# Performance work log

Measured on AMD Instinct MI355X. Metric: run time of the kernel, lower is better.

## Reference

```python
import jax, jax.numpy as jnp
import numpy as np
import math

C_CURV = 1.0          # manifold curvature c
KH = KW = 3
STRIDE = (1, 1)
PADDING = (1, 1)
DILATION = (1, 1)
IN_CH = 64            # includes time channel
OUT_CH = 64           # excludes time channel


def setup_inputs() -> dict:
    key = jax.random.key(0)
    k1, k2, k3 = jax.random.split(key, 3)
    B, H, W = 32, 64, 64
    x = jax.random.normal(k1, (B, H, W, IN_CH), dtype=jnp.float32)
    kk = KH * KW
    lin_in = (IN_CH - 1) * kk + 1  # 568
    stdv = math.sqrt(2.0 / ((IN_CH - 1) * kk))
    weight = jax.random.uniform(k2, (OUT_CH, lin_in), minval=-stdv, maxval=stdv, dtype=jnp.float32)
    bias = jax.random.uniform(k3, (OUT_CH,), minval=-stdv, maxval=stdv, dtype=jnp.float32)
    return {"x": x, "weight": weight, "bias": bias}


def _im2col(x):
    """x: [B,H,W,C] -> gathered patches [B,h_out,w_out,KH,KW,C] (torch Unfold semantics)."""
    B, H, W, C = x.shape
    xp = jnp.pad(x, ((0, 0), (PADDING[0], PADDING[0]), (PADDING[1], PADDING[1]), (0, 0)))
    h_out = (H + 2 * PADDING[0] - DILATION[0] * (KH - 1) - 1) // STRIDE[0] + 1
    w_out = (W + 2 * PADDING[1] - DILATION[1] * (KW - 1) - 1) // STRIDE[1] + 1
    rows = STRIDE[0] * jnp.arange(h_out)[:, None] + DILATION[0] * jnp.arange(KH)[None, :]  # [h_out,KH]
    cols = STRIDE[1] * jnp.arange(w_out)[:, None] + DILATION[1] * jnp.arange(KW)[None, :]  # [w_out,KW]
    g = xp[:, rows[:, None, :, None], cols[None, :, None, :], :]  # [B,h_out,w_out,KH,KW,C]
    return g, h_out, w_out


def reference(x, weight, bias):
    B = x.shape[0]
    kk = KH * KW
    g, h_out, w_out = _im2col(x)
    L = h_out * w_out
    # Time channel (channel 0) over kernel positions, clamped to sqrt(c)
    t = jnp.maximum(g[..., 0].reshape(B, L, kk), jnp.sqrt(jnp.float32(C_CURV)))
    t_rescaled = jnp.sqrt(jnp.sum(t * t, axis=-1, keepdims=True) - (kk - 1) * C_CURV)
    # Space channels in kernel-major, channel-minor order (matches torch reshape/transpose)
    s = g[..., 1:].reshape(B, L, kk * (IN_CH - 1))
    feat = jnp.concatenate([t_rescaled, s], axis=-1)  # [B, L, 568]
    # LorentzLinear: linear on features, recompute time from space norm
    y_space = jnp.einsum('blf,of->blo', feat, weight) + bias
    y_time = jnp.sqrt(jnp.sum(y_space * y_space, axis=-1, keepdims=True) + C_CURV)
    out = jnp.concatenate([y_time, y_space], axis=-1)
    return out.reshape(B, h_out, w_out, OUT_CH + 1)
```

## Files before the change

kernel.cpp:

```cpp
#include <hip/hip_runtime.h>
#include <cstdint>
#include <cstddef>

typedef __attribute__((ext_vector_type(4))) short short4v;
typedef __attribute__((ext_vector_type(8))) short short8v;
typedef __attribute__((ext_vector_type(4))) float floatx4;

#define LIN 568

__device__ __forceinline__ short f32_to_bf16(float f) {
  unsigned u = __builtin_bit_cast(unsigned, f);
  u += 0x7fffu + ((u >> 16) & 1u);
  return (short)(u >> 16);
}
__device__ __forceinline__ float bf16_to_f32(short s) {
  return __builtin_bit_cast(float, ((unsigned)(unsigned short)s) << 16);
}

__global__ void prep_weight(const float* __restrict__ w, short* __restrict__ wfragg) {
  int i = blockIdx.x * 256 + threadIdx.x;
  if (i >= 9 * 2 * 4 * 64 * 8) return;
  int j    = i & 7;
  int lane = (i >> 3) & 63;
  int nb   = (i >> 9) & 3;
  int half = (i >> 11) & 1;
  int tap  = i >> 12;
  int n = nb * 16 + (lane & 15);
  int c = half * 32 + ((lane >> 4) << 3) + j;
  float v = (c == 0) ? 0.0f : w[n * LIN + 1 + tap * 63 + (c - 1)];
  wfragg[i] = f32_to_bf16(v);
}

__launch_bounds__(256, 2)
__global__ void lconv_main(const float* __restrict__ x, const float* __restrict__ w,
                           const float* __restrict__ bias, const short* __restrict__ wfragg,
                           float* __restrict__ out) {
  __shared__ short xt[6 * 66 * 72];

  const int tid = threadIdx.x;
  const int bb = blockIdx.x >> 4;
  const int h0 = (blockIdx.x & 15) << 2;
  const float* xb = x + (size_t)bb * (64 * 64 * 64);

  const int lane = tid & 63;
  const int l15 = lane & 15;
  const int q = lane >> 4;
  const int wv = tid >> 6;

  const short* wfl = wfragg + lane * 8;
  short8v b0[4], b1[4], b2[4];
#pragma unroll
  for (int nb = 0; nb < 4; ++nb) {
    b0[nb] = *(const short8v*)(wfl + 0 * 2048 + nb * 512);
    b1[nb] = *(const short8v*)(wfl + 1 * 2048 + nb * 512);
    b2[nb] = *(const short8v*)(wfl + 2 * 2048 + nb * 512);
  }
  float bj[4], w0j[4];
#pragma unroll
  for (int nb = 0; nb < 4; ++nb) {
    int n = nb * 16 + l15;
    bj[nb] = bias[n];
    w0j[nb] = w[n * LIN];
  }

#pragma unroll
  for (int i = 0; i < 8; ++i) {
    int idx = i * 256 + tid;
    int row = idx >> 9;
    int rem = idx & 511;
    int col = rem >> 3;
    int ch8 = (rem & 7) << 3;
    int h = h0 - 1 + row;
    float4 v0 = {0.f, 0.f, 0.f, 0.f}, v1 = {0.f, 0.f, 0.f, 0.f};
    if ((unsigned)h < 64u) {
      const float* p = xb + ((h * 64 + col) * 64 + ch8);
      v0 = *(const float4*)p;
      v1 = *(const float4*)(p + 4);
    }
    short8v o;
    o[0] = f32_to_bf16(v0.x); o[1] = f32_to_bf16(v0.y);
    o[2] = f32_to_bf16(v0.z); o[3] = f32_to_bf16(v0.w);
    o[4] = f32_to_bf16(v1.x); o[5] = f32_to_bf16(v1.y);
    o[6] = f32_to_bf16(v1.z); o[7] = f32_to_bf16(v1.w);
    *(short8v*)&xt[(row * 66 + col + 1) * 72 + ch8] = o;
  }
  if (tid < 64) {
    int r = tid >> 4;
    int cc = (tid >> 3) & 1;
    int ch8 = (tid & 7) << 3;
    short8v z = {0, 0, 0, 0, 0, 0, 0, 0};
    *(short8v*)&xt[(r * 66 + cc * 65) * 72 + ch8] = z;
  }
  __syncthreads();

#pragma unroll
  for (int i = 8; i < 12; ++i) {
    int idx = i * 256 + tid;
    int row = idx >> 9;
    int rem = idx & 511;
    int col = rem >> 3;
    int ch8 = (rem & 7) << 3;
    int h = h0 - 1 + row;
    float4 v0 = {0.f, 0.f, 0.f, 0.f}, v1 = {0.f, 0.f, 0.f, 0.f};
    if ((unsigned)h < 64u) {
      const float* p = xb + ((h * 64 + col) * 64 + ch8);
      v0 = *(const float4*)p;
      v1 = *(const float4*)(p + 4);
    }
    short8v o;
    o[0] = f32_to_bf16(v0.x); o[1] = f32_to_bf16(v0.y);
    o[2] = f32_to_bf16(v0.z); o[3] = f32_to_bf16(v0.w);
    o[4] = f32_to_bf16(v1.x); o[5] = f32_to_bf16(v1.y);
    o[6] = f32_to_bf16(v1.z); o[7] = f32_to_bf16(v1.w);
    *(short8v*)&xt[(row * 66 + col + 1) * 72 + ch8] = o;
  }
  if (tid < 32) {
    int r = 4 + (tid >> 4);
    int cc = (tid >> 3) & 1;
    int ch8 = (tid & 7) << 3;
    short8v z = {0, 0, 0, 0, 0, 0, 0, 0};
    *(short8v*)&xt[(r * 66 + cc * 65) * 72 + ch8] = z;
  }

  floatx4 acc[4][4];
#pragma unroll
  for (int mb = 0; mb < 4; ++mb)
#pragma unroll
    for (int nb = 0; nb < 4; ++nb) acc[mb][nb] = floatx4{0.f, 0.f, 0.f, 0.f};

  auto do_step = [&](int step) {
    const int tap = step >> 1, half = step & 1;
    const int kh = tap / 3, kw = tap % 3;

    short8v bn[4];
    if (step + 3 < 18) {
#pragma unroll
      for (int nb = 0; nb < 4; ++nb)
        bn[nb] = *(const short8v*)(wfl + (step + 3) * 2048 + nb * 512);
    }

    const short* ab = &xt[((wv + kh) * 66 + kw + l15) * 72 + half * 32 + q * 8];
    short8v a[4];
#pragma unroll
    for (int mb = 0; mb < 4; ++mb)
      a[mb] = *(const short8v*)(ab + mb * 16 * 72);

#pragma unroll
    for (int mb = 0; mb < 4; ++mb) {
#pragma unroll
      for (int nb = 0; nb < 4; ++nb)
        acc[mb][nb] = __builtin_amdgcn_mfma_f32_16x16x32_bf16(a[mb], b0[nb], acc[mb][nb], 0, 0, 0);
    }
#pragma unroll
    for (int nb = 0; nb < 4; ++nb) { b0[nb] = b1[nb]; b1[nb] = b2[nb]; b2[nb] = bn[nb]; }
  };

#pragma unroll
  for (int step = 0; step < 6; ++step) do_step(step);

  __syncthreads();

#pragma unroll
  for (int step = 6; step < 18; ++step) do_step(step);

  float tres_v;
  {
    float ss = 0.f;
#pragma unroll
    for (int dh = 0; dh < 3; ++dh)
#pragma unroll
      for (int dw = 0; dw < 3; ++dw) {
        float tv = bf16_to_f32(xt[((wv + dh) * 66 + lane + dw) * 72]);
        tv = fmaxf(tv, 1.0f);
        ss += tv * tv;
      }
    tres_v = sqrtf(ss - 8.0f);
  }

#pragma unroll
  for (int mb = 0; mb < 4; ++mb) {
#pragma unroll
    for (int r = 0; r < 4; ++r) {
      int pcol = mb * 16 + q * 4 + r;
      float tr = __shfl(tres_v, pcol);
      float v0 = acc[mb][0][r] + bj[0] + tr * w0j[0];
      float v1 = acc[mb][1][r] + bj[1] + tr * w0j[1];
      float v2 = acc[mb][2][r] + bj[2] + tr * w0j[2];
      float v3 = acc[mb][3][r] + bj[3] + tr * w0j[3];
      float ss = v0 * v0 + v1 * v1 + v2 * v2 + v3 * v3;
      ss += __shfl_xor(ss, 1);
      ss += __shfl_xor(ss, 2);
      ss += __shfl_xor(ss, 4);
      ss += __shfl_xor(ss, 8);
      float* ob = out + (size_t)((bb * 64 + h0 + wv) * 64 + pcol) * 65;
      if (l15 == 0) ob[0] = sqrtf(ss + 1.0f);
      ob[1 + l15]  = v0;
      ob[17 + l15] = v1;
      ob[33 + l15] = v2;
      ob[49 + l15] = v3;
    }
  }
}

extern "C" void kernel_launch(void* const* d_in, const int* in_sizes, int n_in,
                              void* d_out, int out_size, void* d_ws, size_t ws_size,
                              hipStream_t stream) {
  const float* x = (const float*)d_in[0];
  const float* w = (const float*)d_in[1];
  const float* b = (const float*)d_in[2];
  float* out = (float*)d_out;
  short* wfragg = (short*)d_ws;

  prep_weight<<<144, 256, 0, stream>>>(w, wfragg);
  lconv_main<<<32 * 16, 256, 0, stream>>>(x, w, b, wfragg, out);
}
```

Measured before the change: 98.81 us.

## Shrink conv tile to two output rows with XOR-swizzled unpadded LDS layout

Each block now computes 2 output rows with 128 threads instead of 4 rows with 256, which doubles the grid and cuts the halo tile to 4 input rows. The padded LDS layout (66 cols x 72 stride) is replaced by an unpadded 64x64 layout that XOR-swizzles channel groups to avoid bank conflicts, and border zeros are applied in registers instead of stored. The weight prefetch depth drops from 3 to 2 stages to save registers, and the load/compute split point is moved. In exchange, the 2-row halo is reloaded more often relative to useful rows (2x instead of 1.5x), and extra masking and index arithmetic are added.

```diff
diff --git a/kernel.cpp b/kernel.cpp
--- a/kernel.cpp
+++ b/kernel.cpp
@@ -2,7 +2,6 @@
 #include <cstdint>
 #include <cstddef>
 
-typedef __attribute__((ext_vector_type(4))) short short4v;
 typedef __attribute__((ext_vector_type(8))) short short8v;
 typedef __attribute__((ext_vector_type(4))) float floatx4;
 
@@ -31,15 +30,15 @@
   wfragg[i] = f32_to_bf16(v);
 }
 
-__launch_bounds__(256, 2)
+__launch_bounds__(128, 3)
 __global__ void lconv_main(const float* __restrict__ x, const float* __restrict__ w,
                            const float* __restrict__ bias, const short* __restrict__ wfragg,
                            float* __restrict__ out) {
-  __shared__ short xt[6 * 66 * 72];
+  __shared__ short xt[4 * 64 * 64];
 
   const int tid = threadIdx.x;
-  const int bb = blockIdx.x >> 4;
-  const int h0 = (blockIdx.x & 15) << 2;
+  const int bb = blockIdx.x >> 5;
+  const int h0 = (blockIdx.x & 31) << 1;
   const float* xb = x + (size_t)bb * (64 * 64 * 64);
 
   const int lane = tid & 63;
@@ -48,12 +47,11 @@
   const int wv = tid >> 6;
 
   const short* wfl = wfragg + lane * 8;
-  short8v b0[4], b1[4], b2[4];
+  short8v b0[4], b1[4];
 #pragma unroll
   for (int nb = 0; nb < 4; ++nb) {
     b0[nb] = *(const short8v*)(wfl + 0 * 2048 + nb * 512);
     b1[nb] = *(const short8v*)(wfl + 1 * 2048 + nb * 512);
-    b2[nb] = *(const short8v*)(wfl + 2 * 2048 + nb * 512);
   }
   float bj[4], w0j[4];
 #pragma unroll
@@ -64,16 +62,16 @@
   }
 
 #pragma unroll
-  for (int i = 0; i < 8; ++i) {
-    int idx = i * 256 + tid;
+  for (int i = 0; i < 12; ++i) {
+    int idx = i * 128 + tid;
     int row = idx >> 9;
     int rem = idx & 511;
     int col = rem >> 3;
-    int ch8 = (rem & 7) << 3;
+    int g   = rem & 7;
     int h = h0 - 1 + row;
     float4 v0 = {0.f, 0.f, 0.f, 0.f}, v1 = {0.f, 0.f, 0.f, 0.f};
     if ((unsigned)h < 64u) {
-      const float* p = xb + ((h * 64 + col) * 64 + ch8);
+      const float* p = xb + ((h * 64 + col) * 64 + g * 8);
       v0 = *(const float4*)p;
       v1 = *(const float4*)(p + 4);
     }
@@ -82,28 +80,19 @@
     o[2] = f32_to_bf16(v0.z); o[3] = f32_to_bf16(v0.w);
     o[4] = f32_to_bf16(v1.x); o[5] = f32_to_bf16(v1.y);
     o[6] = f32_to_bf16(v1.z); o[7] = f32_to_bf16(v1.w);
-    *(short8v*)&xt[(row * 66 + col + 1) * 72 + ch8] = o;
-  }
-  if (tid < 64) {
-    int r = tid >> 4;
-    int cc = (tid >> 3) & 1;
-    int ch8 = (tid & 7) << 3;
-    short8v z = {0, 0, 0, 0, 0, 0, 0, 0};
-    *(short8v*)&xt[(r * 66 + cc * 65) * 72 + ch8] = z;
+    *(short8v*)&xt[((row * 64 + col) << 6) + ((g ^ (col & 7)) << 3)] = o;
   }
   __syncthreads();
 
 #pragma unroll
-  for (int i = 8; i < 12; ++i) {
-    int idx = i * 256 + tid;
-    int row = idx >> 9;
-    int rem = idx & 511;
-    int col = rem >> 3;
-    int ch8 = (rem & 7) << 3;
-    int h = h0 - 1 + row;
+  for (int i = 0; i < 4; ++i) {
+    int idx = i * 128 + tid;
+    int col = idx >> 3;
+    int g   = idx & 7;
+    int h = h0 + 2;
     float4 v0 = {0.f, 0.f, 0.f, 0.f}, v1 = {0.f, 0.f, 0.f, 0.f};
     if ((unsigned)h < 64u) {
-      const float* p = xb + ((h * 64 + col) * 64 + ch8);
+      const float* p = xb + ((h * 64 + col) * 64 + g * 8);
       v0 = *(const float4*)p;
       v1 = *(const float4*)(p + 4);
     }
@@ -112,14 +101,7 @@
     o[2] = f32_to_bf16(v0.z); o[3] = f32_to_bf16(v0.w);
     o[4] = f32_to_bf16(v1.x); o[5] = f32_to_bf16(v1.y);
     o[6] = f32_to_bf16(v1.z); o[7] = f32_to_bf16(v1.w);
-    *(short8v*)&xt[(row * 66 + col + 1) * 72 + ch8] = o;
-  }
-  if (tid < 32) {
-    int r = 4 + (tid >> 4);
-    int cc = (tid >> 3) & 1;
-    int ch8 = (tid & 7) << 3;
-    short8v z = {0, 0, 0, 0, 0, 0, 0, 0};
-    *(short8v*)&xt[(r * 66 + cc * 65) * 72 + ch8] = z;
+    *(short8v*)&xt[((3 * 64 + col) << 6) + ((g ^ (col & 7)) << 3)] = o;
   }
 
   floatx4 acc[4][4];
@@ -133,17 +115,24 @@
     const int kh = tap / 3, kw = tap % 3;
 
     short8v bn[4];
-    if (step + 3 < 18) {
+    if (step + 2 < 18) {
 #pragma unroll
       for (int nb = 0; nb < 4; ++nb)
-        bn[nb] = *(const short8v*)(wfl + (step + 3) * 2048 + nb * 512);
-    }
-
-    const short* ab = &xt[((wv + kh) * 66 + kw + l15) * 72 + half * 32 + q * 8];
+        bn[nb] = *(const short8v*)(wfl + (step + 2) * 2048 + nb * 512);
+    }
+
+    const int rb = (wv + kh) << 6;
+    const int cb = l15 + kw - 1;
+    const int ch = (half << 2) + q;
     short8v a[4];
 #pragma unroll
-    for (int mb = 0; mb < 4; ++mb)
-      a[mb] = *(const short8v*)(ab + mb * 16 * 72);
+    for (int mb = 0; mb < 4; ++mb) {
+      int col = (cb + mb * 16) & 63;
+      a[mb] = *(const short8v*)&xt[((rb + col) << 6) + ((ch ^ (col & 7)) << 3)];
+    }
+    short8v z = {0, 0, 0, 0, 0, 0, 0, 0};
+    if (kw == 0 && l15 == 0) a[0] = z;
+    if (kw == 2 && l15 == 15) a[3] = z;
 
 #pragma unroll
     for (int mb = 0; mb < 4; ++mb) {
@@ -152,16 +141,16 @@
         acc[mb][nb] = __builtin_amdgcn_mfma_f32_16x16x32_bf16(a[mb], b0[nb], acc[mb][nb], 0, 0, 0);
     }
 #pragma unroll
-    for (int nb = 0; nb < 4; ++nb) { b0[nb] = b1[nb]; b1[nb] = b2[nb]; b2[nb] = bn[nb]; }
+    for (int nb = 0; nb < 4; ++nb) { b0[nb] = b1[nb]; b1[nb] = bn[nb]; }
   };
 
 #pragma unroll
-  for (int step = 0; step < 6; ++step) do_step(step);
+  for (int step = 0; step < 12; ++step) do_step(step);
 
   __syncthreads();
 
 #pragma unroll
-  for (int step = 6; step < 18; ++step) do_step(step);
+  for (int step = 12; step < 18; ++step) do_step(step);
 
   float tres_v;
   {
@@ -170,7 +159,10 @@
     for (int dh = 0; dh < 3; ++dh)
 #pragma unroll
       for (int dw = 0; dw < 3; ++dw) {
-        float tv = bf16_to_f32(xt[((wv + dh) * 66 + lane + dw) * 72]);
+        int c = lane + dw - 1;
+        int cc = c & 63;
+        float tv = bf16_to_f32(xt[(((wv + dh) * 64 + cc) << 6) + ((cc & 7) << 3)]);
+        tv = ((unsigned)c < 64u) ? tv : 0.f;
         tv = fmaxf(tv, 1.0f);
         ss += tv * tv;
       }
@@ -212,5 +204,5 @@
   short* wfragg = (short*)d_ws;
 
   prep_weight<<<144, 256, 0, stream>>>(w, wfragg);
-  lconv_main<<<32 * 16, 256, 0, stream>>>(x, w, b, wfragg, out);
-}
+  lconv_main<<<32 * 32, 128, 0, stream>>>(x, w, b, wfragg, out);
+}
```

Measured after the change: 106.2 us. 7.5% more time.
